# Kernel tuning notes

Hardware: AMD Instinct MI355X
Metric: run time of the kernel (lower is better)

## Reference

```python
import jax, jax.numpy as jnp
import numpy as np

B, S, E, HEAD = 8, 2048, 512, 64  # head_size = embeddings_dims // no_of_heads = 512 // 8


def setup_inputs() -> dict:
    key = jax.random.key(0)
    kx, kq, kk, kv, kl = jax.random.split(key, 5)
    x = jax.random.normal(kx, (B, S, E), dtype=jnp.float32)
    # Linear(512 -> 64, bias=False); store as [E, HEAD] so y = x @ W
    Wq = jax.random.normal(kq, (E, HEAD), dtype=jnp.float32) * (E ** -0.5)
    Wk = jax.random.normal(kk, (E, HEAD), dtype=jnp.float32) * (E ** -0.5)
    Wv = jax.random.normal(kv, (E, HEAD), dtype=jnp.float32) * (E ** -0.5)
    # Realistic padding mask: 1 for first `length` tokens, 0 after.
    lengths = jax.random.randint(kl, (B,), S // 2, S + 1)
    mask = (jnp.arange(S)[None, :] < lengths[:, None]).astype(jnp.int32)
    return {"x": x, "Wq": Wq, "Wk": Wk, "Wv": Wv, "mask": mask}


def reference(x, Wq, Wk, Wv, mask):
    # q, k, v: [B, S, HEAD]
    q = x @ Wq
    k = x @ Wk
    v = x @ Wv
    # scores: [B, S, S], scaled by head_size**-0.5 (k.shape[-1] in the original)
    scores = jnp.einsum('bqd,bkd->bqk', q, k) * (HEAD ** -0.5)
    causal = jnp.tril(jnp.ones((S, S), dtype=bool))            # [S, S]
    keep = (mask[:, None, :] != 0) & causal[None, :, :]        # padding mask broadcast over query rows, then causal
    scores = jnp.where(keep, scores, -jnp.inf)
    attn = jax.nn.softmax(scores, axis=-1)                     # [B, S, S]
    out = attn @ v                                             # [B, S, HEAD]
    return out
```

## Files before the change

### kernel.cpp

```cpp
#include <hip/hip_runtime.h>

#define BB 8
#define SS 2048
#define EE 512
#define HD 64
#define CHUNK 256
#define KT 64
#define NCH 8
#define PST 72
#define TST 72
#define XRS 40
#define XKB 640
#define NITEMS 1152

typedef __attribute__((ext_vector_type(8))) short bf16x8;
typedef __attribute__((ext_vector_type(4))) float f32x4;

static __device__ __forceinline__ unsigned short f2bf(float f) {
    unsigned u = __builtin_bit_cast(unsigned, f);
    u = (u + 0x7fffu + ((u >> 16) & 1u)) >> 16;
    return (unsigned short)u;
}
static __device__ __forceinline__ unsigned short f2bf_trunc(float f) {
    return (unsigned short)(__builtin_bit_cast(unsigned, f) >> 16);
}
static __device__ __forceinline__ float bf2f(unsigned short h) {
    unsigned u = ((unsigned)h) << 16;
    return __builtin_bit_cast(float, u);
}

__global__ __launch_bounds__(256) void pack_w_kernel(
    const float* __restrict__ Wq, const float* __restrict__ Wk, const float* __restrict__ Wv,
    unsigned short* __restrict__ Wt, int* __restrict__ tickets) {
    if (blockIdx.x == 0 && threadIdx.x == 0) atomicExch(tickets, 0);
    int tid = blockIdx.x * 256 + threadIdx.x;
    if (tid >= 3 * EE * HD) return;
    int w_idx = tid / (EE * HD);
    int rem = tid % (EE * HD);
    int kk = rem / HD, n = rem % HD;
    const float* Wsrc = (w_idx == 0) ? Wq : ((w_idx == 1) ? Wk : Wv);
    float val = Wsrc[kk * HD + n];
    if (w_idx == 0) val *= 0.125f;
    int kb = kk >> 5, kr = kk & 31, quad = kr >> 3, j = kr & 7;
    int t = n >> 4, c = n & 15;
    int lane = quad * 16 + c;
    Wt[w_idx * (EE * HD) + ((kb * 4 + t) * 64 + lane) * 8 + j] = f2bf(val);
}

__global__ __launch_bounds__(256) void qkv_kernel(
    const float* __restrict__ x,
    const unsigned short* __restrict__ Wt,
    unsigned short* __restrict__ q,
    unsigned short* __restrict__ k,
    unsigned short* __restrict__ vT) {
    __shared__ __align__(16) unsigned short Xs[16 * XKB];
    const int tid = threadIdx.x;
    const int lane = tid & 63;
    const int t = tid >> 6;
    const int c = lane & 15, quad = lane >> 4;
    const int r0 = blockIdx.x * 16;

    const float* xt = x + (size_t)r0 * EE;
#pragma unroll
    for (int i = 0; i < 8; ++i) {
        int fi = i * 256 + tid;
        int e4 = fi * 4;
        float4 v4 = *(const float4*)(xt + e4);
        int row = e4 >> 9, col = e4 & 511;
        int kb = col >> 5, cc = col & 31;
        ushort4 pk;
        pk.x = f2bf(v4.x); pk.y = f2bf(v4.y); pk.z = f2bf(v4.z); pk.w = f2bf(v4.w);
        *(ushort4*)(&Xs[kb * XKB + row * XRS + cc]) = pk;
    }
    __syncthreads();

    f32x4 acc[3];
    for (int m = 0; m < 3; ++m) acc[m] = (f32x4){0.f, 0.f, 0.f, 0.f};

    const unsigned short* wbase0 = Wt + t * 512 + lane * 8;
#pragma unroll
    for (int kb = 0; kb < EE / 32; ++kb) {
        bf16x8 afrag = *(const bf16x8*)(&Xs[kb * XKB + c * XRS + quad * 8]);
        const unsigned short* wb = wbase0 + kb * 2048;
#pragma unroll
        for (int m = 0; m < 3; ++m) {
            bf16x8 bfrag = *(const bf16x8*)(wb + m * (EE * HD));
            acc[m] = __builtin_amdgcn_mfma_f32_16x16x32_bf16(afrag, bfrag, acc[m], 0, 0, 0);
        }
    }

    const int col = t * 16 + c;
    for (int r = 0; r < 4; ++r) {
        int row = r0 + quad * 4 + r;
        q[(size_t)row * HD + col] = f2bf(acc[0][r]);
        k[(size_t)row * HD + col] = f2bf(acc[1][r]);
    }
    {
        int row = r0 + quad * 4;
        int b_ = row >> 11, sb = row & (SS - 1);
        ushort4 pk;
        pk.x = f2bf(acc[2][0]); pk.y = f2bf(acc[2][1]);
        pk.z = f2bf(acc[2][2]); pk.w = f2bf(acc[2][3]);
        *(ushort4*)(vT + ((size_t)b_ * HD + col) * SS + sb) = pk;
    }
}

__global__ __launch_bounds__(256) void attn_kernel(
    const unsigned short* __restrict__ q,
    const unsigned short* __restrict__ k,
    const unsigned short* __restrict__ vT,
    const int* __restrict__ mask,
    unsigned short* __restrict__ po,
    float* __restrict__ pl,
    int* __restrict__ tickets,
    float* __restrict__ out) {
    __shared__ __align__(16) unsigned short Ks[2][64 * TST];
    __shared__ __align__(16) unsigned short Vs[2][64 * TST];
    __shared__ __align__(16) unsigned short Ps[4][16 * PST];
    __shared__ int tkt;
    const int tid = threadIdx.x;
    const int lane = tid & 63, wave = tid >> 6;
    const int c = lane & 15, quad = lane >> 4;

    for (;;) {
        __syncthreads();
        if (tid == 0) tkt = atomicAdd(tickets, 1);
        __syncthreads();
        int t = tkt;
        if (t >= NITEMS) break;
        t = NITEMS - 1 - t;
        const int b_ = t / 144;
        int r = t % 144;
        int g = 0;
        while (2 * (g + 1) * (g + 2) <= r) ++g;
        int rr = r - 2 * g * (g + 1);
        const int qb = 4 * g + rr / (g + 1);
        const int cx = rr % (g + 1);
        const int kstart = cx * CHUNK;
        const int kend = min(kstart + CHUNK, qb * 64 + 64);
        const int ntiles = (kend - kstart) >> 6;
        const int r0 = qb * 64 + wave * 16;
        const int nch_active = qb / 4 + 1;

        const unsigned short* qb_p = q + (size_t)b_ * SS * HD;
        const unsigned short* kb_p = k + (size_t)b_ * SS * HD;
        const unsigned short* vb = vT + (size_t)b_ * HD * SS;
        const int* mb = mask + b_ * SS;

        bf16x8 aq0 = *(const bf16x8*)(qb_p + (size_t)(r0 + c) * HD + quad * 8);
        bf16x8 aq1 = *(const bf16x8*)(qb_p + (size_t)(r0 + c) * HD + 32 + quad * 8);

        f32x4 o[4];
        for (int tt = 0; tt < 4; ++tt) o[tt] = (f32x4){0.f, 0.f, 0.f, 0.f};
        float l_i[4] = {0.f, 0.f, 0.f, 0.f};

        auto stage = [&](int buf, int k0) {
            const unsigned short* ksrc = kb_p + (size_t)k0 * HD;
            unsigned short* kd = &Ks[buf][0];
            unsigned short* vd = &Vs[buf][0];
#pragma unroll
            for (int rnd = 0; rnd < 2; ++rnd) {
                int e = (rnd * 256 + tid) * 8;
                int krow = e >> 6, kcol = e & 63;
                *(bf16x8*)(kd + krow * TST + kcol) = *(const bf16x8*)(ksrc + e);
                int t8 = rnd * 256 + tid;
                int vr = t8 >> 3, vc = (t8 & 7) * 8;
                *(bf16x8*)(vd + vr * TST + vc) = *(const bf16x8*)(vb + (size_t)vr * SS + k0 + vc);
            }
        };

        stage(0, kstart);
        for (int kt = 0; kt < ntiles; ++kt) {
            __syncthreads();
            const unsigned short* ks = &Ks[kt & 1][0];
            const unsigned short* vs = &Vs[kt & 1][0];
            const int k0 = kstart + kt * KT;
            bf16x8 kf[4][2];
#pragma unroll
            for (int kg = 0; kg < 4; ++kg) {
                kf[kg][0] = *(const bf16x8*)(ks + (kg * 16 + c) * TST + quad * 8);
                kf[kg][1] = *(const bf16x8*)(ks + (kg * 16 + c) * TST + 32 + quad * 8);
            }
            if (kt + 1 < ntiles) stage((kt + 1) & 1, k0 + KT);
            const bool fullc = (k0 + KT <= r0);
            float p[4][4];
#pragma unroll
            for (int kg = 0; kg < 4; ++kg) {
                f32x4 accs = (f32x4){0.f, 0.f, 0.f, 0.f};
                accs = __builtin_amdgcn_mfma_f32_16x16x32_bf16(aq0, kf[kg][0], accs, 0, 0, 0);
                accs = __builtin_amdgcn_mfma_f32_16x16x32_bf16(aq1, kf[kg][1], accs, 0, 0, 0);
                int key = k0 + kg * 16 + c;
                bool mk = (mb[key] != 0);
                for (int rr2 = 0; rr2 < 4; ++rr2) {
                    int row = r0 + quad * 4 + rr2;
                    bool keep = mk && (fullc || key <= row);
                    float e = __expf(fminf(accs[rr2], 80.f));
                    float pe = keep ? e : 0.f;
                    p[kg][rr2] = pe;
                    l_i[rr2] += pe;
                }
            }
            unsigned short* pbuf = &Ps[wave][0];
#pragma unroll
            for (int kg = 0; kg < 4; ++kg)
                for (int rr2 = 0; rr2 < 4; ++rr2)
                    pbuf[(quad * 4 + rr2) * PST + kg * 16 + c] = f2bf_trunc(p[kg][rr2]);
            bf16x8 pa0 = *(const bf16x8*)(pbuf + c * PST + quad * 8);
            bf16x8 pa1 = *(const bf16x8*)(pbuf + c * PST + 32 + quad * 8);
#pragma unroll
            for (int tt = 0; tt < 4; ++tt) {
                bf16x8 bv0 = *(const bf16x8*)(vs + (tt * 16 + c) * TST + quad * 8);
                bf16x8 bv1 = *(const bf16x8*)(vs + (tt * 16 + c) * TST + 32 + quad * 8);
                o[tt] = __builtin_amdgcn_mfma_f32_16x16x32_bf16(pa0, bv0, o[tt], 0, 0, 0);
                o[tt] = __builtin_amdgcn_mfma_f32_16x16x32_bf16(pa1, bv1, o[tt], 0, 0, 0);
            }
        }

        for (int rr2 = 0; rr2 < 4; ++rr2) {
            float s = l_i[rr2];
            s += __shfl_xor(s, 1);
            s += __shfl_xor(s, 2);
            s += __shfl_xor(s, 4);
            s += __shfl_xor(s, 8);
            l_i[rr2] = s;
        }

        if (nch_active == 1) {
            for (int rr2 = 0; rr2 < 4; ++rr2) {
                int row = qb * 64 + wave * 16 + quad * 4 + rr2;
                float l = l_i[rr2];
                float inv = (l > 0.f) ? 1.f / l : 0.f;
                for (int tt = 0; tt < 4; ++tt)
                    out[((size_t)b_ * SS + row) * HD + tt * 16 + c] = o[tt][rr2] * inv;
            }
            continue;
        }

        const size_t base = (size_t)(b_ * 32 + qb) * NCH + cx;
        for (int rr2 = 0; rr2 < 4; ++rr2) {
            int rl = wave * 16 + quad * 4 + rr2;
            float l = l_i[rr2];
            float inv = (l > 0.f) ? 1.f / l : 0.f;
            for (int tt = 0; tt < 4; ++tt)
                po[base * 4096 + (size_t)rl * 64 + tt * 16 + c] = f2bf(o[tt][rr2] * inv);
            if (c == 0) pl[base * 64 + rl] = l;
        }
    }
}

__global__ __launch_bounds__(256) void combine_kernel(
    const unsigned short* __restrict__ po,
    const float* __restrict__ pl,
    float* __restrict__ out) {
    int t = blockIdx.x * 256 + threadIdx.x;
    if (t >= BB * (SS - 256) * HD) return;
    int d = t & 63;
    int rg = t >> 6;
    int b_ = rg / (SS - 256);
    int row = 256 + rg % (SS - 256);
    int qb = row >> 6, rl = row & 63;
    int nch = row / CHUNK + 1;
    size_t base = (size_t)(b_ * 32 + qb) * NCH;
    float L = 0.f, acc = 0.f;
    for (int c = 0; c < nch; ++c) {
        float l = pl[(base + c) * 64 + rl];
        L += l;
        acc += l * bf2f(po[(base + c) * 4096 + (size_t)rl * 64 + d]);
    }
    out[((size_t)b_ * SS + row) * HD + d] = (L > 0.f) ? acc / L : 0.f;
}

extern "C" void kernel_launch(void* const* d_in, const int* in_sizes, int n_in,
                              void* d_out, int out_size, void* d_ws, size_t ws_size,
                              hipStream_t stream) {
    const float* x = (const float*)d_in[0];
    const float* Wq = (const float*)d_in[1];
    const float* Wk = (const float*)d_in[2];
    const float* Wv = (const float*)d_in[3];
    const int* mask = (const int*)d_in[4];
    float* out = (float*)d_out;

    unsigned short* ws = (unsigned short*)d_ws;
    unsigned short* Wt = ws;
    unsigned short* q = Wt + 3 * EE * HD;
    unsigned short* kk = q + (size_t)BB * SS * HD;
    unsigned short* vT = kk + (size_t)BB * SS * HD;
    unsigned short* po = vT + (size_t)BB * SS * HD;
    float* pl = (float*)(po + (size_t)BB * 32 * NCH * 4096);
    int* tickets = (int*)(pl + (size_t)BB * 32 * NCH * 64);

    pack_w_kernel<<<dim3((3 * EE * HD + 255) / 256), dim3(256), 0, stream>>>(Wq, Wk, Wv, Wt, tickets);
    qkv_kernel<<<dim3(BB * SS / 16), dim3(256), 0, stream>>>(x, Wt, q, kk, vT);
    attn_kernel<<<dim3(768), dim3(256), 0, stream>>>(q, kk, vT, mask, po, pl, tickets, out);
    combine_kernel<<<dim3((BB * (SS - 256) * HD + 255) / 256), dim3(256), 0, stream>>>(po, pl, out);
}
```

Before: 125.9 us.

## Process 128-row query blocks per work item to reuse staged K/V tiles

Each work item now covers 128 query rows instead of 64, with each wave computing two 16-row sub-tiles against the same staged K and V tile in shared memory. This halves the number of work items and the K/V global loads and staging per query row. Partial outputs are still written in the 64-row layout the combine kernel expects. Launch bounds now request 3 blocks per SM. The cost is more registers per wave and coarser scheduling granularity, which may worsen load balance in the causal work distribution.

```diff
diff --git a/kernel.cpp b/kernel.cpp
--- a/kernel.cpp
+++ b/kernel.cpp
@@ -11,7 +11,7 @@
 #define TST 72
 #define XRS 40
 #define XKB 640
-#define NITEMS 1152
+#define NITEMS 576
 
 typedef __attribute__((ext_vector_type(8))) short bf16x8;
 typedef __attribute__((ext_vector_type(4))) float f32x4;
@@ -105,7 +105,7 @@
     }
 }
 
-__global__ __launch_bounds__(256) void attn_kernel(
+__global__ __launch_bounds__(256, 3) void attn_kernel(
     const unsigned short* __restrict__ q,
     const unsigned short* __restrict__ k,
     const unsigned short* __restrict__ vT,
@@ -129,30 +129,40 @@
         int t = tkt;
         if (t >= NITEMS) break;
         t = NITEMS - 1 - t;
-        const int b_ = t / 144;
-        int r = t % 144;
+        const int b_ = t / 72;
+        int r = t % 72;
         int g = 0;
-        while (2 * (g + 1) * (g + 2) <= r) ++g;
-        int rr = r - 2 * g * (g + 1);
-        const int qb = 4 * g + rr / (g + 1);
+        while ((g + 1) * (g + 2) <= r) ++g;
+        int rr = r - g * (g + 1);
+        const int Q = 2 * g + rr / (g + 1);
         const int cx = rr % (g + 1);
         const int kstart = cx * CHUNK;
-        const int kend = min(kstart + CHUNK, qb * 64 + 64);
+        const int kend = min(kstart + CHUNK, Q * 128 + 128);
         const int ntiles = (kend - kstart) >> 6;
-        const int r0 = qb * 64 + wave * 16;
-        const int nch_active = qb / 4 + 1;
+        const int nch_active = Q / 2 + 1;
+        const int r0 = Q * 128 + wave * 32;
 
         const unsigned short* qb_p = q + (size_t)b_ * SS * HD;
         const unsigned short* kb_p = k + (size_t)b_ * SS * HD;
         const unsigned short* vb = vT + (size_t)b_ * HD * SS;
         const int* mb = mask + b_ * SS;
 
-        bf16x8 aq0 = *(const bf16x8*)(qb_p + (size_t)(r0 + c) * HD + quad * 8);
-        bf16x8 aq1 = *(const bf16x8*)(qb_p + (size_t)(r0 + c) * HD + 32 + quad * 8);
-
-        f32x4 o[4];
-        for (int tt = 0; tt < 4; ++tt) o[tt] = (f32x4){0.f, 0.f, 0.f, 0.f};
-        float l_i[4] = {0.f, 0.f, 0.f, 0.f};
+        bf16x8 aq[2][2];
+#pragma unroll
+        for (int rt = 0; rt < 2; ++rt) {
+            const unsigned short* qrow = qb_p + (size_t)(r0 + rt * 16 + c) * HD + quad * 8;
+            aq[rt][0] = *(const bf16x8*)(qrow);
+            aq[rt][1] = *(const bf16x8*)(qrow + 32);
+        }
+
+        f32x4 o[2][4];
+        float l_i[2][4];
+#pragma unroll
+        for (int rt = 0; rt < 2; ++rt)
+            for (int tt = 0; tt < 4; ++tt) {
+                o[rt][tt] = (f32x4){0.f, 0.f, 0.f, 0.f};
+                l_i[rt][tt] = 0.f;
+            }
 
         auto stage = [&](int buf, int k0) {
             const unsigned short* ksrc = kb_p + (size_t)k0 * HD;
@@ -182,69 +192,80 @@
                 kf[kg][1] = *(const bf16x8*)(ks + (kg * 16 + c) * TST + 32 + quad * 8);
             }
             if (kt + 1 < ntiles) stage((kt + 1) & 1, k0 + KT);
-            const bool fullc = (k0 + KT <= r0);
-            float p[4][4];
-#pragma unroll
-            for (int kg = 0; kg < 4; ++kg) {
-                f32x4 accs = (f32x4){0.f, 0.f, 0.f, 0.f};
-                accs = __builtin_amdgcn_mfma_f32_16x16x32_bf16(aq0, kf[kg][0], accs, 0, 0, 0);
-                accs = __builtin_amdgcn_mfma_f32_16x16x32_bf16(aq1, kf[kg][1], accs, 0, 0, 0);
-                int key = k0 + kg * 16 + c;
-                bool mk = (mb[key] != 0);
+#pragma unroll
+            for (int rt = 0; rt < 2; ++rt) {
+                const int rbase = r0 + rt * 16;
+                const bool fullc = (k0 + KT <= rbase);
+                float p[4][4];
+#pragma unroll
+                for (int kg = 0; kg < 4; ++kg) {
+                    f32x4 accs = (f32x4){0.f, 0.f, 0.f, 0.f};
+                    accs = __builtin_amdgcn_mfma_f32_16x16x32_bf16(aq[rt][0], kf[kg][0], accs, 0, 0, 0);
+                    accs = __builtin_amdgcn_mfma_f32_16x16x32_bf16(aq[rt][1], kf[kg][1], accs, 0, 0, 0);
+                    int key = k0 + kg * 16 + c;
+                    bool mk = (mb[key] != 0);
+                    for (int rr2 = 0; rr2 < 4; ++rr2) {
+                        int row = rbase + quad * 4 + rr2;
+                        bool keep = mk && (fullc || key <= row);
+                        float e = __expf(fminf(accs[rr2], 80.f));
+                        float pe = keep ? e : 0.f;
+                        p[kg][rr2] = pe;
+                        l_i[rt][rr2] += pe;
+                    }
+                }
+                unsigned short* pbuf = &Ps[wave][0];
+#pragma unroll
+                for (int kg = 0; kg < 4; ++kg)
+                    for (int rr2 = 0; rr2 < 4; ++rr2)
+                        pbuf[(quad * 4 + rr2) * PST + kg * 16 + c] = f2bf_trunc(p[kg][rr2]);
+                bf16x8 pa0 = *(const bf16x8*)(pbuf + c * PST + quad * 8);
+                bf16x8 pa1 = *(const bf16x8*)(pbuf + c * PST + 32 + quad * 8);
+#pragma unroll
+                for (int tt = 0; tt < 4; ++tt) {
+                    bf16x8 bv0 = *(const bf16x8*)(vs + (tt * 16 + c) * TST + quad * 8);
+                    bf16x8 bv1 = *(const bf16x8*)(vs + (tt * 16 + c) * TST + 32 + quad * 8);
+                    o[rt][tt] = __builtin_amdgcn_mfma_f32_16x16x32_bf16(pa0, bv0, o[rt][tt], 0, 0, 0);
+                    o[rt][tt] = __builtin_amdgcn_mfma_f32_16x16x32_bf16(pa1, bv1, o[rt][tt], 0, 0, 0);
+                }
+            }
+        }
+
+#pragma unroll
+        for (int rt = 0; rt < 2; ++rt)
+            for (int rr2 = 0; rr2 < 4; ++rr2) {
+                float s = l_i[rt][rr2];
+                s += __shfl_xor(s, 1);
+                s += __shfl_xor(s, 2);
+                s += __shfl_xor(s, 4);
+                s += __shfl_xor(s, 8);
+                l_i[rt][rr2] = s;
+            }
+
+        if (nch_active == 1) {
+#pragma unroll
+            for (int rt = 0; rt < 2; ++rt)
                 for (int rr2 = 0; rr2 < 4; ++rr2) {
-                    int row = r0 + quad * 4 + rr2;
-                    bool keep = mk && (fullc || key <= row);
-                    float e = __expf(fminf(accs[rr2], 80.f));
-                    float pe = keep ? e : 0.f;
-                    p[kg][rr2] = pe;
-                    l_i[rr2] += pe;
+                    int row = r0 + rt * 16 + quad * 4 + rr2;
+                    float l = l_i[rt][rr2];
+                    float inv = (l > 0.f) ? 1.f / l : 0.f;
+                    for (int tt = 0; tt < 4; ++tt)
+                        out[((size_t)b_ * SS + row) * HD + tt * 16 + c] = o[rt][tt][rr2] * inv;
                 }
-            }
-            unsigned short* pbuf = &Ps[wave][0];
-#pragma unroll
-            for (int kg = 0; kg < 4; ++kg)
-                for (int rr2 = 0; rr2 < 4; ++rr2)
-                    pbuf[(quad * 4 + rr2) * PST + kg * 16 + c] = f2bf_trunc(p[kg][rr2]);
-            bf16x8 pa0 = *(const bf16x8*)(pbuf + c * PST + quad * 8);
-            bf16x8 pa1 = *(const bf16x8*)(pbuf + c * PST + 32 + quad * 8);
-#pragma unroll
-            for (int tt = 0; tt < 4; ++tt) {
-                bf16x8 bv0 = *(const bf16x8*)(vs + (tt * 16 + c) * TST + quad * 8);
-                bf16x8 bv1 = *(const bf16x8*)(vs + (tt * 16 + c) * TST + 32 + quad * 8);
-                o[tt] = __builtin_amdgcn_mfma_f32_16x16x32_bf16(pa0, bv0, o[tt], 0, 0, 0);
-                o[tt] = __builtin_amdgcn_mfma_f32_16x16x32_bf16(pa1, bv1, o[tt], 0, 0, 0);
-            }
+            continue;
         }
 
-        for (int rr2 = 0; rr2 < 4; ++rr2) {
-            float s = l_i[rr2];
-            s += __shfl_xor(s, 1);
-            s += __shfl_xor(s, 2);
-            s += __shfl_xor(s, 4);
-            s += __shfl_xor(s, 8);
-            l_i[rr2] = s;
-        }
-
-        if (nch_active == 1) {
+#pragma unroll
+        for (int rt = 0; rt < 2; ++rt)
             for (int rr2 = 0; rr2 < 4; ++rr2) {
-                int row = qb * 64 + wave * 16 + quad * 4 + rr2;
-                float l = l_i[rr2];
+                int row_abs = r0 + rt * 16 + quad * 4 + rr2;
+                int qb_i = row_abs >> 6, rl = row_abs & 63;
+                size_t base = (size_t)(b_ * 32 + qb_i) * NCH + cx;
+                float l = l_i[rt][rr2];
                 float inv = (l > 0.f) ? 1.f / l : 0.f;
                 for (int tt = 0; tt < 4; ++tt)
-                    out[((size_t)b_ * SS + row) * HD + tt * 16 + c] = o[tt][rr2] * inv;
-            }
-            continue;
-        }
-
-        const size_t base = (size_t)(b_ * 32 + qb) * NCH + cx;
-        for (int rr2 = 0; rr2 < 4; ++rr2) {
-            int rl = wave * 16 + quad * 4 + rr2;
-            float l = l_i[rr2];
-            float inv = (l > 0.f) ? 1.f / l : 0.f;
-            for (int tt = 0; tt < 4; ++tt)
-                po[base * 4096 + (size_t)rl * 64 + tt * 16 + c] = f2bf(o[tt][rr2] * inv);
-            if (c == 0) pl[base * 64 + rl] = l;
-        }
+                    po[base * 4096 + (size_t)rl * 64 + tt * 16 + c] = f2bf(o[rt][tt][rr2] * inv);
+                if (c == 0) pl[base * 64 + rl] = l;
+            }
     }
 }
 
```

Result: no change. 124.5 us (-1.1%).
